# Kernel optimization log

Measured on AMD Instinct MI355X. Metric: run time of the kernel, lower is better.

The kernel has to match this reference:

```python
import jax, jax.numpy as jnp
import numpy as np

EPS_NORM = 1e-12   # torch F.normalize eps
EPS_SQ = 1e-12     # floor on squared distance before sqrt


def _l2_normalize(x):
    # matches torch F.normalize(x, p=2, dim=1, eps=1e-12)
    n = jnp.sqrt(jnp.sum(x * x, axis=-1, keepdims=True))
    return x / jnp.maximum(n, EPS_NORM)


def setup_inputs() -> dict:
    key = jax.random.key(0)
    k1, k2, k3 = jax.random.split(key, 3)
    N, D, C = 16384, 2048, 8192
    features = jax.random.normal(k1, (N, D), dtype=jnp.float32)
    # prototypes initialized N(0, 10) as in the module
    prototypes = jax.random.normal(k2, (C, D), dtype=jnp.float32) * 10.0
    distance_scale = jnp.ones((1,), dtype=jnp.float32)
    return {"features": features, "prototypes": prototypes, "distance_scale": distance_scale}


def reference(features, prototypes, distance_scale):
    # Both operands are L2-normalized, so ||f - p||^2 = 2 - 2 <f, p>.
    f = _l2_normalize(features)      # [N, D]
    p = _l2_normalize(prototypes)    # [C, D]
    sim = jnp.einsum('nd,cd->nc', f, p)                 # [N, C]
    sq = jnp.maximum(2.0 - 2.0 * sim, EPS_SQ)
    distances = jnp.abs(distance_scale[0]) * jnp.sqrt(sq)
    return -distances
```

## Files before the change

kernel.cpp:

```cpp
#include <hip/hip_runtime.h>
#include <stdint.h>


#define K_DIM 2048
#define BM 256
#define BN 256
#define BK 64
#define NT (K_DIM / BK)

typedef short bf16x8 __attribute__((ext_vector_type(8)));
typedef float f32x4 __attribute__((ext_vector_type(4)));

__device__ __forceinline__ unsigned short f32_to_bf16(float f) {
  unsigned u = __float_as_uint(f);
  unsigned r = 0x7FFFu + ((u >> 16) & 1u);
  return (unsigned short)((u + r) >> 16);
}

__global__ __launch_bounds__(256) void norm_rows_wave(
    const float* __restrict__ in, unsigned short* __restrict__ out,
    int nrows) {
  const int lane = threadIdx.x & 63;
  const int wid = (blockIdx.x << 2) + (threadIdx.x >> 6);
  const int nw = gridDim.x << 2;
  for (int row = wid; row < nrows; row += nw) {
    const float4* rp = (const float4*)(in + (size_t)row * K_DIM);
    float4 v[8];
#pragma unroll
    for (int j = 0; j < 8; ++j) v[j] = rp[lane + (j << 6)];
    float ss = 0.0f;
#pragma unroll
    for (int j = 0; j < 8; ++j)
      ss += v[j].x * v[j].x + v[j].y * v[j].y + v[j].z * v[j].z +
            v[j].w * v[j].w;
#pragma unroll
    for (int off = 32; off > 0; off >>= 1) ss += __shfl_xor(ss, off, 64);
    const float inv = 1.0f / fmaxf(sqrtf(ss), 1e-12f);
    ushort4* op = (ushort4*)(out + (size_t)row * K_DIM);
#pragma unroll
    for (int j = 0; j < 8; ++j) {
      ushort4 o;
      o.x = f32_to_bf16(v[j].x * inv);
      o.y = f32_to_bf16(v[j].y * inv);
      o.z = f32_to_bf16(v[j].z * inv);
      o.w = f32_to_bf16(v[j].w * inv);
      op[lane + (j << 6)] = o;
    }
  }
}

__device__ __forceinline__ void async_load16(const void* gptr, uint32_t lds_off,
                                             void* lds_base) {
  typedef __attribute__((address_space(3))) uint32_t lds_u32_t;
  typedef const __attribute__((address_space(1))) uint32_t glb_u32_t;
  glb_u32_t* g = reinterpret_cast<glb_u32_t*>(reinterpret_cast<uintptr_t>(gptr));
  lds_u32_t* l = reinterpret_cast<lds_u32_t*>(
      (uint32_t)(reinterpret_cast<uintptr_t>(lds_base) + lds_off));
  __builtin_amdgcn_global_load_lds(g, l, 16, 0, 0);
}

__device__ __forceinline__ void stage_a(const unsigned short* gA,
                                        unsigned short* lds_, int wave, int buf,
                                        int half, int tt) {
  const unsigned short* s = gA + (size_t)(half * 128) * K_DIM + (size_t)tt * BK;
  uint32_t d = (uint32_t)(buf * 65536 + half * 16384 + wave * 1024);
  async_load16(s, d, lds_);
  async_load16(s + (size_t)64 * K_DIM, d + 8192u, lds_);
}
__device__ __forceinline__ void stage_b(const unsigned short* gB,
                                        unsigned short* lds_, int wave, int buf,
                                        int half, int tt) {
  const unsigned short* s = gB + (size_t)(half * 128) * K_DIM + (size_t)tt * BK;
  uint32_t d = (uint32_t)(buf * 65536 + 32768 + half * 16384 + wave * 1024);
  async_load16(s, d, lds_);
  async_load16(s + (size_t)64 * K_DIM, d + 8192u, lds_);
}

__device__ __forceinline__ void ld_a(bf16x8 (&dst)[4][2],
                                     const unsigned short* lds_, int bufe,
                                     int mh, int wm, int frow, int lxe) {
#pragma unroll
  for (int fi = 0; fi < 4; ++fi)
#pragma unroll
    for (int ks = 0; ks < 2; ++ks)
      dst[fi][ks] = *(const bf16x8*)(lds_ + bufe +
                                     (wm * 128 + mh * 64 + fi * 16 + frow) * 64 +
                                     (lxe ^ (ks << 5)));
}
__device__ __forceinline__ void ld_b(bf16x8 (&dst)[2][2],
                                     const unsigned short* lds_, int bufe,
                                     int nh, int wn, int frow, int lxe) {
#pragma unroll
  for (int fj = 0; fj < 2; ++fj)
#pragma unroll
    for (int ks = 0; ks < 2; ++ks)
      dst[fj][ks] = *(const bf16x8*)(lds_ + bufe + 16384 +
                                     (wn * 64 + nh * 32 + fj * 16 + frow) * 64 +
                                     (lxe ^ (ks << 5)));
}

__device__ __forceinline__ void mfma_quad(f32x4 (&acc)[8][4],
                                          const bf16x8 (&af)[4][2],
                                          const bf16x8 (&bf)[2][2], int mh,
                                          int nh) {
#pragma unroll
  for (int fi = 0; fi < 4; ++fi)
#pragma unroll
    for (int fj = 0; fj < 2; ++fj) {
      f32x4 c = acc[mh * 4 + fi][nh * 2 + fj];
      c = __builtin_amdgcn_mfma_f32_16x16x32_bf16(af[fi][0], bf[fj][0], c, 0, 0, 0);
      c = __builtin_amdgcn_mfma_f32_16x16x32_bf16(af[fi][1], bf[fj][1], c, 0, 0, 0);
      acc[mh * 4 + fi][nh * 2 + fj] = c;
    }
}

#define KTILE(BUF, OBUF, T)                                                   \
  do {                                                                        \
    const int _stb1 = ((T) + 1 < NT) ? (T) + 1 : NT - 1;                      \
    const int _st2 = ((T) + 2 < NT) ? (T) + 2 : NT - 1;                       \
                                                                 \
    ld_a(a0, lds, (BUF)*32768, 0, wm, frow, lxe);                             \
    ld_b(b0, lds, (BUF)*32768, 0, wn, frow, lxe);                             \
    stage_b(gB, lds, wave, OBUF, 1, _stb1);                                   \
    __builtin_amdgcn_s_barrier();                                             \
    asm volatile("s_waitcnt lgkmcnt(0)" ::: "memory");                        \
    __builtin_amdgcn_s_setprio(1);                                            \
    mfma_quad(acc, a0, b0, 0, 0);                                             \
    __builtin_amdgcn_s_setprio(0);                                            \
    __builtin_amdgcn_s_barrier();                                             \
                                                                 \
    ld_a(a1, lds, (BUF)*32768, 1, wm, frow, lxe);                             \
    stage_a(gA, lds, wave, BUF, 0, _st2);                                     \
    __builtin_amdgcn_s_barrier();                                             \
    asm volatile("s_waitcnt lgkmcnt(0)" ::: "memory");                        \
    __builtin_amdgcn_s_setprio(1);                                            \
    mfma_quad(acc, a1, b0, 1, 0);                                             \
    __builtin_amdgcn_s_setprio(0);                                            \
    __builtin_amdgcn_s_barrier();                                             \
                                                                 \
    ld_b(b1, lds, (BUF)*32768, 1, wn, frow, lxe);                             \
    stage_a(gA, lds, wave, BUF, 1, _st2);                                     \
    __builtin_amdgcn_s_barrier();                                             \
    asm volatile("s_waitcnt lgkmcnt(0)" ::: "memory");                        \
    __builtin_amdgcn_s_setprio(1);                                            \
    mfma_quad(acc, a1, b1, 1, 1);                                             \
    __builtin_amdgcn_s_setprio(0);                                            \
    __builtin_amdgcn_s_barrier();                                             \
                                                                 \
    stage_b(gB, lds, wave, BUF, 0, _st2);                                     \
    asm volatile("s_waitcnt vmcnt(6)" ::: "memory");                          \
    __builtin_amdgcn_s_barrier();                                             \
    __builtin_amdgcn_s_setprio(1);                                            \
    mfma_quad(acc, a0, b1, 0, 1);                                             \
    __builtin_amdgcn_s_setprio(0);                                            \
    __builtin_amdgcn_s_barrier();                                             \
  } while (0)

__global__ __launch_bounds__(512, 2) void gemm_bt_dist(
    const unsigned short* __restrict__ A, const unsigned short* __restrict__ B,
    float* __restrict__ Out, const float* __restrict__ scale_ptr, int N,
    int C) {
  __shared__ __align__(16) unsigned short lds[65536];

  const int tid = threadIdx.x;
  const int wave = tid >> 6;
  const int lane = tid & 63;
  const int wm = wave >> 2;
  const int wn = wave & 3;

  const int nwg = gridDim.x;
  const int orig = blockIdx.x;
  const int tiles_n = C / BN;
  int tm, tn;
  if (nwg == 2048 && tiles_n == 32) {
    const int x = orig & 7;
    const int l = orig >> 3;
    tm = (x << 3) + ((l & 63) >> 3);
    tn = ((l >> 6) << 3) + (l & 7);
  } else {
    const int swz = (orig & 7) * (nwg >> 3) + (orig >> 3);
    tm = swz / tiles_n;
    tn = swz % tiles_n;
  }
  const int m0 = tm * BM;
  const int n0 = tn * BN;

  const int srow = tid >> 3;
  const int swslot = (tid & 7) ^ (srow & 7);
  const unsigned short* gA = A + (size_t)(m0 + srow) * K_DIM + swslot * 8;
  const unsigned short* gB = B + (size_t)(n0 + srow) * K_DIM + swslot * 8;

  const int frow = lane & 15;
  const int lxe = (((lane >> 4) ^ (lane & 7)) << 3);

  f32x4 acc[8][4] = {};
  bf16x8 a0[4][2], a1[4][2], b0[2][2], b1[2][2];

  stage_a(gA, lds, wave, 0, 0, 0);
  stage_a(gA, lds, wave, 0, 1, 0);
  stage_b(gB, lds, wave, 0, 0, 0);
  stage_b(gB, lds, wave, 0, 1, 0);
  stage_a(gA, lds, wave, 1, 0, 1);
  stage_a(gA, lds, wave, 1, 1, 1);
  stage_b(gB, lds, wave, 1, 0, 1);
  asm volatile("s_waitcnt vmcnt(6)" ::: "memory");
  __builtin_amdgcn_s_barrier();

#pragma unroll 1
  for (int t = 0; t < NT; t += 2) {
    KTILE(0, 1, t);
    KTILE(1, 0, t + 1);
  }

  asm volatile("s_waitcnt vmcnt(0)" ::: "memory");

  const float s = fabsf(scale_ptr[0]);
  const int ocol0 = n0 + wn * 64 + (lane & 15);
  const int orow0 = m0 + wm * 128 + ((lane >> 4) << 2);
#pragma unroll
  for (int ai = 0; ai < 8; ++ai) {
#pragma unroll
    for (int bj = 0; bj < 4; ++bj) {
      f32x4 v = acc[ai][bj];
#pragma unroll
      for (int r = 0; r < 4; ++r) {
        float sq = fmaxf(2.0f - 2.0f * v[r], 1e-12f);
        Out[(size_t)(orow0 + ai * 16 + r) * C + (ocol0 + bj * 16)] =
            -s * sqrtf(sq);
      }
    }
  }
}

extern "C" void kernel_launch(void* const* d_in, const int* in_sizes, int n_in,
                              void* d_out, int out_size, void* d_ws,
                              size_t ws_size, hipStream_t stream) {
  const float* feats = (const float*)d_in[0];
  const float* protos = (const float*)d_in[1];
  const float* dscale = (const float*)d_in[2];
  float* out = (float*)d_out;

  const int N = in_sizes[0] / K_DIM;
  const int C = in_sizes[1] / K_DIM;

  unsigned short* fb = (unsigned short*)d_ws;
  unsigned short* pb = fb + (size_t)N * K_DIM;

  norm_rows_wave<<<2048, 256, 0, stream>>>(feats, fb, N);
  norm_rows_wave<<<2048, 256, 0, stream>>>(protos, pb, C);

  const int nwg = (N / BM) * (C / BN);
  gemm_bt_dist<<<dim3(nwg), 512, 0, stream>>>(fb, pb, out, dscale, N, C);
}
```

Baseline: 1.076 ms.

## Merge K-tile phases and stage epilogue through LDS for coalesced stores

The main-loop schedule drops from four barrier-separated MFMA phases per K tile to two. Both A fragment loads are issued up front, and all global staging for the tile after next is grouped into the second phase, which halves the barriers. The epilogue now computes the distances, writes them into swizzled shared memory in two halves, and then stores them to global memory with coalesced 16-byte vector writes. Before, each lane wrote scattered 4-byte values. The cost is more live fragment registers, fewer chances to overlap loads with MFMA, and extra LDS traffic and syncs in the epilogue.

```diff
diff --git a/kernel.cpp b/kernel.cpp
--- a/kernel.cpp
+++ b/kernel.cpp
@@ -118,39 +118,28 @@
   do {                                                                        \
     const int _stb1 = ((T) + 1 < NT) ? (T) + 1 : NT - 1;                      \
     const int _st2 = ((T) + 2 < NT) ? (T) + 2 : NT - 1;                       \
-                                                                 \
+                                        \
     ld_a(a0, lds, (BUF)*32768, 0, wm, frow, lxe);                             \
     ld_b(b0, lds, (BUF)*32768, 0, wn, frow, lxe);                             \
+    ld_a(a1, lds, (BUF)*32768, 1, wm, frow, lxe);                             \
     stage_b(gB, lds, wave, OBUF, 1, _stb1);                                   \
     __builtin_amdgcn_s_barrier();                                             \
     asm volatile("s_waitcnt lgkmcnt(0)" ::: "memory");                        \
     __builtin_amdgcn_s_setprio(1);                                            \
     mfma_quad(acc, a0, b0, 0, 0);                                             \
-    __builtin_amdgcn_s_setprio(0);                                            \
-    __builtin_amdgcn_s_barrier();                                             \
-                                                                 \
-    ld_a(a1, lds, (BUF)*32768, 1, wm, frow, lxe);                             \
-    stage_a(gA, lds, wave, BUF, 0, _st2);                                     \
-    __builtin_amdgcn_s_barrier();                                             \
-    asm volatile("s_waitcnt lgkmcnt(0)" ::: "memory");                        \
-    __builtin_amdgcn_s_setprio(1);                                            \
     mfma_quad(acc, a1, b0, 1, 0);                                             \
     __builtin_amdgcn_s_setprio(0);                                            \
     __builtin_amdgcn_s_barrier();                                             \
-                                                                 \
+                                        \
     ld_b(b1, lds, (BUF)*32768, 1, wn, frow, lxe);                             \
+    stage_a(gA, lds, wave, BUF, 0, _st2);                                     \
     stage_a(gA, lds, wave, BUF, 1, _st2);                                     \
+    stage_b(gB, lds, wave, BUF, 0, _st2);                                     \
+    asm volatile("s_waitcnt vmcnt(6)" ::: "memory");                          \
     __builtin_amdgcn_s_barrier();                                             \
     asm volatile("s_waitcnt lgkmcnt(0)" ::: "memory");                        \
     __builtin_amdgcn_s_setprio(1);                                            \
     mfma_quad(acc, a1, b1, 1, 1);                                             \
-    __builtin_amdgcn_s_setprio(0);                                            \
-    __builtin_amdgcn_s_barrier();                                             \
-                                                                 \
-    stage_b(gB, lds, wave, BUF, 0, _st2);                                     \
-    asm volatile("s_waitcnt vmcnt(6)" ::: "memory");                          \
-    __builtin_amdgcn_s_barrier();                                             \
-    __builtin_amdgcn_s_setprio(1);                                            \
     mfma_quad(acc, a0, b1, 0, 1);                                             \
     __builtin_amdgcn_s_setprio(0);                                            \
     __builtin_amdgcn_s_barrier();                                             \
@@ -213,22 +202,46 @@
   }
 
   asm volatile("s_waitcnt vmcnt(0)" ::: "memory");
+  __syncthreads();
 
   const float s = fabsf(scale_ptr[0]);
-  const int ocol0 = n0 + wn * 64 + (lane & 15);
-  const int orow0 = m0 + wm * 128 + ((lane >> 4) << 2);
-#pragma unroll
-  for (int ai = 0; ai < 8; ++ai) {
-#pragma unroll
-    for (int bj = 0; bj < 4; ++bj) {
-      f32x4 v = acc[ai][bj];
-#pragma unroll
-      for (int r = 0; r < 4; ++r) {
-        float sq = fmaxf(2.0f - 2.0f * v[r], 1e-12f);
-        Out[(size_t)(orow0 + ai * 16 + r) * C + (ocol0 + bj * 16)] =
-            -s * sqrtf(sq);
+  float* lf = (float*)lds;
+  const int l16 = lane >> 4;
+  const int l15 = lane & 15;
+  const int rbase = tid >> 4;
+  const int cslot = (tid & 15) << 4;
+#pragma unroll
+  for (int c = 0; c < 2; ++c) {
+#pragma unroll
+    for (int fi = 0; fi < 4; ++fi) {
+#pragma unroll
+      for (int bj = 0; bj < 4; ++bj) {
+        f32x4 v = acc[c * 4 + fi][bj];
+        const int col = wn * 64 + bj * 16 + l15;
+#pragma unroll
+        for (int r = 0; r < 4; ++r) {
+          const int rl = wm * 64 + fi * 16 + l16 * 4 + r;
+          const int sw = ((rl & 3) << 2) ^ (((rl >> 2) & 3) << 3);
+          const float sq = fmaxf(2.0f - 2.0f * v[r], 1e-12f);
+          lf[rl * 256 + (col ^ sw)] = -s * sqrtf(sq);
+        }
       }
     }
+    __syncthreads();
+#pragma unroll
+    for (int p = 0; p < 4; ++p) {
+      const int rl = rbase + 32 * p;
+      const int sw = ((rl & 3) << 2) ^ (((rl >> 2) & 3) << 3);
+      const int grow = m0 + ((rl >> 6) << 7) + c * 64 + (rl & 63);
+      float* outp = Out + (size_t)grow * C + n0;
+#pragma unroll
+      for (int q = 0; q < 4; ++q) {
+        const int colw = cslot + (q << 2);
+        f32x4 val = *(const f32x4*)(lf + rl * 256 + (colw ^ sw));
+        *(f32x4*)(outp + colw) = val;
+      }
+    }
+    __syncthreads();
   }
 }
 
```

Result: slower. 1.207 ms (+12.2%).
